# Performance work log

Hardware: AMD Instinct MI355X
Metric: run time of the kernel (lower is better)

The kernel has to match this reference:

```python
import jax, jax.numpy as jnp
import numpy as np

HEADS = 6
EPS = 1e-5

def conv1x1(x, w):
    return jax.lax.conv_general_dilated(x, w, (1, 1), 'VALID',
        dimension_numbers=('NCHW', 'OIHW', 'NCHW'))

def dwconv3x3(x, w):
    # depthwise 3x3, padding 1; w: [C,1,3,3]
    return jax.lax.conv_general_dilated(x, w, (1, 1), ((1, 1), (1, 1)),
        dimension_numbers=('NCHW', 'OIHW', 'NCHW'), feature_group_count=x.shape[1])

def layernorm(x, w, b):
    # WithBias LayerNorm over channel dim (applied per pixel)
    mu = x.mean(axis=1, keepdims=True)
    var = ((x - mu) ** 2).mean(axis=1, keepdims=True)
    return (x - mu) * jax.lax.rsqrt(var + EPS) * w[None, :, None, None] + b[None, :, None, None]

def l2norm(t):
    # matches torch F.normalize(dim=-1): norm clamped at 1e-12
    n = jnp.sqrt(jnp.sum(t * t, axis=-1, keepdims=True))
    return t / jnp.maximum(n, 1e-12)

def attention(x, f, qkv_w, dw_w, proj_w, temp):
    xin = x + f
    b, c, h, w = xin.shape
    qkv = dwconv3x3(conv1x1(xin, qkv_w), dw_w)
    q, k, v = jnp.split(qkv, 3, axis=1)
    hd = c // HEADS
    q = l2norm(q.reshape(b, HEADS, hd, h * w))
    k = l2norm(k.reshape(b, HEADS, hd, h * w))
    v = v.reshape(b, HEADS, hd, h * w)
    attn = jnp.einsum('bhcn,bhdn->bhcd', q, k) * temp[None]  # [b,H,hd,hd]
    attn = jax.nn.softmax(attn, axis=-1)
    out = jnp.einsum('bhcd,bhdn->bhcn', attn, v).reshape(b, c, h, w)
    return conv1x1(out, proj_w)

def ffn(x, in_w, dw_w, out_w):
    x = conv1x1(x, in_w)
    x1, x2 = jnp.split(dwconv3x3(x, dw_w), 2, axis=1)
    return conv1x1(jax.nn.gelu(x1, approximate=False) * x2, out_w)

def setup_inputs() -> dict:
    key = jax.random.key(0)
    B, C, H, W = 2, 96, 256, 256
    HID = int(C * 2.66)  # 255
    ks = jax.random.split(key, 32)
    p = lambda k, shp: (0.02 * jax.random.normal(k, shp, dtype=jnp.float32))
    d = {
        'Fw': jax.random.normal(ks[0], (B, C, H, W), dtype=jnp.float32),
        'F0_c': jax.random.normal(ks[1], (B, C, H, W), dtype=jnp.float32),
        'Kd': jax.random.normal(ks[2], (B, C, H, W), dtype=jnp.float32),
        'ln1_w': jnp.ones((C,), jnp.float32), 'ln1_b': jnp.zeros((C,), jnp.float32),
        'a1_qkv_w': p(ks[3], (3 * C, C, 1, 1)), 'a1_dw_w': p(ks[4], (3 * C, 1, 3, 3)),
        'a1_proj_w': p(ks[5], (C, C, 1, 1)), 'a1_temp': jnp.ones((HEADS, 1, 1), jnp.float32),
        'ln2_w': jnp.ones((C,), jnp.float32), 'ln2_b': jnp.zeros((C,), jnp.float32),
        'f1_in_w': p(ks[6], (2 * HID, C, 1, 1)), 'f1_dw_w': p(ks[7], (2 * HID, 1, 3, 3)),
        'f1_out_w': p(ks[8], (C, HID, 1, 1)),
        'ln3_w': jnp.ones((C,), jnp.float32), 'ln3_b': jnp.zeros((C,), jnp.float32),
        'a2_qkv_w': p(ks[9], (3 * C, C, 1, 1)), 'a2_dw_w': p(ks[10], (3 * C, 1, 3, 3)),
        'a2_proj_w': p(ks[11], (C, C, 1, 1)), 'a2_temp': jnp.ones((HEADS, 1, 1), jnp.float32),
        'ln4_w': jnp.ones((C,), jnp.float32), 'ln4_b': jnp.zeros((C,), jnp.float32),
        'f2_in_w': p(ks[12], (2 * HID, C, 1, 1)), 'f2_dw_w': p(ks[13], (2 * HID, 1, 3, 3)),
        'f2_out_w': p(ks[14], (C, HID, 1, 1)),
    }
    return d

def reference(Fw, F0_c, Kd, ln1_w, ln1_b, a1_qkv_w, a1_dw_w, a1_proj_w, a1_temp,
              ln2_w, ln2_b, f1_in_w, f1_dw_w, f1_out_w,
              ln3_w, ln3_b, a2_qkv_w, a2_dw_w, a2_proj_w, a2_temp,
              ln4_w, ln4_b, f2_in_w, f2_dw_w, f2_out_w):
    x = Fw + attention(layernorm(Fw, ln1_w, ln1_b), F0_c, a1_qkv_w, a1_dw_w, a1_proj_w, a1_temp)
    x = x + ffn(layernorm(x, ln2_w, ln2_b), f1_in_w, f1_dw_w, f1_out_w)
    x = x + attention(layernorm(x, ln3_w, ln3_b), Kd, a2_qkv_w, a2_dw_w, a2_proj_w, a2_temp)
    x = x + ffn(layernorm(x, ln4_w, ln4_b), f2_in_w, f2_dw_w, f2_out_w)
    return x
```

## Files before the change

### kernel.cpp

```cpp
#include <hip/hip_runtime.h>
#include <math.h>

using u16 = unsigned short;
using u32 = unsigned int;
typedef __attribute__((ext_vector_type(8))) short bf16x8;
typedef __attribute__((ext_vector_type(4))) float f32x4;
typedef __attribute__((ext_vector_type(16))) float f32x16;

#define NPLANE 65536
#define BELEMS ((size_t)6291456)
#define ASTR   ((size_t)33423360)
#define BSTR   ((size_t)18874368)

__device__ __forceinline__ float bf2f(u16 u) { return __uint_as_float(((u32)u) << 16); }
__device__ __forceinline__ u16 f2bf(float f) {
  if (!__builtin_isfinite(f)) return (u16)0x5F80;
  u32 u = __float_as_uint(f);
  return (u16)((u + 0x7fffu + ((u >> 16) & 1u)) >> 16);
}
__device__ __forceinline__ float4 cvt4(ushort4 v) {
  return make_float4(bf2f(v.x), bf2f(v.y), bf2f(v.z), bf2f(v.w));
}

union U16x8 { uint4 u4; bf16x8 v; u16 s[8]; };

__global__ void k_detect(const u16* __restrict__ p, u32* __restrict__ flag) {
  if (blockIdx.x == 0 && threadIdx.x == 0) *flag = (p[0] == (u16)0x3F80) ? 0u : 1u;
}

__device__ __forceinline__ float ldf(const void* p, int i, bool f32) {
  return f32 ? ((const float*)p)[i] : bf2f(((const u16*)p)[i]);
}

__global__ __launch_bounds__(256) void k_cvt_all(
    const void* p0, const void* p1, const void* p2, const void* p3,
    const void* p4, const void* p5, const void* p6, const void* p7,
    const void* p8, const void* p9, const void* p10, const void* p11,
    const void* p12, const void* p13, const void* p14, const void* p15,
    float* __restrict__ dst, const u32* __restrict__ fl)
{
  const int i = blockIdx.x * 256 + threadIdx.x;
  if (i >= 33576) return;
  const bool xf = (*fl != 0);
  const void* s; int o;
  if      (i < 2592)  { s = p0;  o = i; }
  else if (i < 7182)  { s = p1;  o = i - 2592; }
  else if (i < 9774)  { s = p2;  o = i - 7182; }
  else if (i < 14364) { s = p3;  o = i - 9774; }
  else if (i < 23580) { s = p4;  o = i - 14364; }
  else if (i < 32796) { s = p5;  o = i - 23580; }
  else if (i < 32802) { s = p6;  o = i - 32796; }
  else if (i < 32808) { s = p7;  o = i - 32802; }
  else if (i < 32904) { s = p8;  o = i - 32808; }
  else if (i < 33000) { s = p9;  o = i - 32904; }
  else if (i < 33096) { s = p10; o = i - 33000; }
  else if (i < 33192) { s = p11; o = i - 33096; }
  else if (i < 33288) { s = p12; o = i - 33192; }
  else if (i < 33384) { s = p13; o = i - 33288; }
  else if (i < 33480) { s = p14; o = i - 33384; }
  else                { s = p15; o = i - 33480; }
  dst[i] = ldf(s, o, xf);
}

__global__ __launch_bounds__(256) void k_wprep_all(
    const void* q1, const void* i1, const void* o1,
    const void* q2, const void* i2, const void* o2,
    u16* __restrict__ wbuf, const u32* __restrict__ fl)
{
  const int idx = blockIdx.x * 256 + threadIdx.x;
  if (idx >= 215040) return;
  const bool xf = (*fl != 0);
  const void* s; int local, M, Kr, Kpad;
  if      (idx < 27648)  { s = q1; local = idx;          M = 288; Kr = 96;  Kpad = 96;  }
  else if (idx < 82944)  { s = i1; local = idx - 27648;  M = 510; Kr = 96;  Kpad = 96;  }
  else if (idx < 107520) { s = o1; local = idx - 82944;  M = 96;  Kr = 255; Kpad = 256; }
  else if (idx < 135168) { s = q2; local = idx - 107520; M = 288; Kr = 96;  Kpad = 96;  }
  else if (idx < 190464) { s = i2; local = idx - 135168; M = 510; Kr = 96;  Kpad = 96;  }
  else                   { s = o2; local = idx - 190464; M = 96;  Kr = 255; Kpad = 256; }
  const int m = local / Kpad, k = local - m * Kpad;
  u16 v = 0;
  if (m < M && k < Kr) v = f2bf(ldf(s, m * Kr + k, xf));
  wbuf[idx] = v;
}

__global__ __launch_bounds__(256) void k_lnp(
    const void* __restrict__ x, const u32* __restrict__ xfl,
    const void* __restrict__ f, const u32* __restrict__ ffl,
    const float* __restrict__ lnw, const float* __restrict__ lnb,
    u16* __restrict__ xT)
{
  __shared__ float xin[96 * 64];
  __shared__ float fin[96 * 64];
  __shared__ float ps[256], pq[256];
  __shared__ float mu[64], rsd[64];
  const int tid = threadIdx.x;
  const int pix0 = blockIdx.x * 64;
  const int z = blockIdx.z;
  const size_t eb = (size_t)z * BELEMS;
  u16* xTo = xT + (size_t)z * BSTR;
  const bool xf = xfl && (*xfl != 0);
  const bool ff = ffl && (*ffl != 0);

#pragma unroll
  for (int i = 0; i < 6; ++i) {
    const int u = tid + i * 256;
    const int c = u >> 4, p4 = (u & 15) << 2;
    const size_t base = eb + (size_t)c * NPLANE + pix0 + p4;
    const float4 v = xf ? *(const float4*)((const float*)x + base)
                        : cvt4(*(const ushort4*)((const u16*)x + base));
    *(float4*)(xin + c * 64 + p4) = v;
    if (f) {
      const float4 fv = ff ? *(const float4*)((const float*)f + base)
                           : cvt4(*(const ushort4*)((const u16*)f + base));
      *(float4*)(fin + c * 64 + p4) = fv;
    }
  }
  __syncthreads();
  {
    const int p = tid & 63, qq = tid >> 6;
    float s = 0.f, q = 0.f;
    const int c0 = qq * 24;
#pragma unroll 8
    for (int c = c0; c < c0 + 24; ++c) {
      const float v = xin[c * 64 + p];
      s += v; q += v * v;
    }
    ps[tid] = s; pq[tid] = q;
  }
  __syncthreads();
  if (tid < 64) {
    const float s = ps[tid] + ps[tid + 64] + ps[tid + 128] + ps[tid + 192];
    const float q = pq[tid] + pq[tid + 64] + pq[tid + 128] + pq[tid + 192];
    const float m = s * (1.f / 96.f);
    mu[tid] = m;
    rsd[tid] = rsqrtf(fmaxf(q * (1.f / 96.f) - m * m, 0.f) + 1e-5f);
  }
  __syncthreads();
#pragma unroll
  for (int i = 0; i < 6; ++i) {
    const int u = tid + i * 256;
    const int c = u >> 4, p4 = (u & 15) << 2;
    const float4 v = *(const float4*)(xin + c * 64 + p4);
    const float w = lnw[c], b = lnb[c];
    float o0 = (v.x - mu[p4 + 0]) * rsd[p4 + 0] * w + b;
    float o1 = (v.y - mu[p4 + 1]) * rsd[p4 + 1] * w + b;
    float o2 = (v.z - mu[p4 + 2]) * rsd[p4 + 2] * w + b;
    float o3 = (v.w - mu[p4 + 3]) * rsd[p4 + 3] * w + b;
    if (f) {
      const float4 fv = *(const float4*)(fin + c * 64 + p4);
      o0 += fv.x; o1 += fv.y; o2 += fv.z; o3 += fv.w;
    }
    *(float4*)(xin + c * 64 + p4) = make_float4(o0, o1, o2, o3);
  }
  __syncthreads();
#pragma unroll
  for (int i = 0; i < 3; ++i) {
    const int u = tid + i * 256;
    const int px = u / 12, q = u - px * 12;
    U16x8 pk;
#pragma unroll
    for (int e = 0; e < 8; ++e) pk.s[e] = f2bf(xin[(q * 8 + e) * 64 + px]);
    *(uint4*)(xTo + (size_t)(pix0 + px) * 96 + q * 8) = pk.u4;
  }
}

__global__ __launch_bounds__(256) void k_gemm_bt(
    const u16* __restrict__ BT, size_t bts, const u16* __restrict__ A,
    int OC, u16* __restrict__ out, size_t ots)
{
  __shared__ u16 Bs[128 * 104];
  const int t = threadIdx.x;
  const int oc0 = blockIdx.x * 96;
  const int n0 = blockIdx.y * 128;
  const int z = blockIdx.z;
  const u16* BTz = BT + (size_t)z * bts;
  u16* outz = out + (size_t)z * ots;
  const int l = t & 63, wid = t >> 6, wm = wid >> 1, wn = wid & 1;

  const uint4* src = (const uint4*)(BTz + (size_t)n0 * 96);
#pragma unroll
  for (int i = 0; i < 6; ++i) {
    const int u = t + i * 256;
    const int r = u / 12, q = u - r * 12;
    *(uint4*)(Bs + r * 104 + q * 8) = src[u];
  }
  __syncthreads();

  f32x4 acc[3][4];
#pragma unroll
  for (int m = 0; m < 3; ++m)
#pragma unroll
    for (int n = 0; n < 4; ++n) acc[m][n] = (f32x4){0.f, 0.f, 0.f, 0.f};

#pragma unroll
  for (int ks = 0; ks < 3; ++ks) {
    const int kk = (ks << 5) + ((l >> 4) << 3);
    U16x8 a[3], b[4];
#pragma unroll
    for (int m = 0; m < 3; ++m)
      a[m].u4 = *(const uint4*)(A + (size_t)(oc0 + wm * 48 + m * 16 + (l & 15)) * 96 + kk);
#pragma unroll
    for (int ns = 0; ns < 4; ++ns)
      b[ns].u4 = *(const uint4*)(Bs + (wn * 64 + ns * 16 + (l & 15)) * 104 + kk);
#pragma unroll
    for (int m = 0; m < 3; ++m)
#pragma unroll
      for (int ns = 0; ns < 4; ++ns)
        acc[m][ns] = __builtin_amdgcn_mfma_f32_16x16x32_bf16(a[m].v, b[ns].v, acc[m][ns], 0, 0, 0);
  }

  __syncthreads();
  u16* ct = Bs;
#pragma unroll
  for (int m = 0; m < 3; ++m) {
    const int rl = wm * 48 + m * 16 + ((l >> 4) << 2);
#pragma unroll
    for (int ns = 0; ns < 4; ++ns) {
      const int nl = wn * 64 + ns * 16 + (l & 15);
#pragma unroll
      for (int r = 0; r < 4; ++r) ct[(rl + r) * 136 + nl] = f2bf(acc[m][ns][r]);
    }
  }
  __syncthreads();
#pragma unroll
  for (int i = 0; i < 6; ++i) {
    const int u = t + i * 256;
    const int r = u >> 4, q = u & 15;
    if (oc0 + r < OC) {
      const uint4 pk = *(const uint4*)(ct + r * 136 + q * 8);
      *(uint4*)(outz + (size_t)(oc0 + r) * NPLANE + n0 + q * 8) = pk;
    }
  }
}

__global__ __launch_bounds__(256) void k_gemm(
    const u16* __restrict__ xsrc, size_t xzs, const u16* __restrict__ A, int azs,
    int K, int Kpad, int OC,
    const void* __restrict__ res, const u32* __restrict__ rfl,
    void* __restrict__ out, const u32* __restrict__ ofl)
{
  __shared__ uint4 Bt[128 * 16];
  const int t = threadIdx.x;
  const int p = t & 127, h = t >> 7;
  const int oc0 = blockIdx.x * 96;
  const int n0 = blockIdx.y * 128;
  const int z = blockIdx.z;
  const u16* xz = xsrc + (size_t)z * xzs;
  const u16* Az = A + (size_t)z * (size_t)azs;
  const size_t eb = (size_t)z * BELEMS;
  const int nglob = n0 + p;
  const int l = t & 63, wid = t >> 6, wm = wid >> 1, wn = wid & 1;

  f32x4 acc[3][4];
#pragma unroll
  for (int m = 0; m < 3; ++m)
#pragma unroll
    for (int n = 0; n < 4; ++n) acc[m][n] = (f32x4){0.f, 0.f, 0.f, 0.f};

  for (int kb = 0; kb < K; kb += 128) {
    if (kb) __syncthreads();
    const int kc = min(128, K - kb);
    const int U = (kc + 7) >> 3;
    const int uh = U >> 1;
    for (int j = 0; j < uh; ++j) {
      const int u = h * uh + j;
      const int cb = kb + u * 8;
      U16x8 pk;
#pragma unroll
      for (int e = 0; e < 8; ++e) {
        const int c = cb + e;
        pk.s[e] = (c < K) ? xz[(size_t)c * NPLANE + nglob] : (u16)0;
      }
      Bt[p * 16 + (u ^ (p & 7))] = pk.u4;
    }
    __syncthreads();
    const int nks = (kc + 31) >> 5;
    for (int ks = 0; ks < nks; ++ks) {
      U16x8 a[3], b[4];
      const int kk = kb + ks * 32 + ((l >> 4) << 3);
#pragma unroll
      for (int m = 0; m < 3; ++m) {
        const int row = oc0 + wm * 48 + m * 16 + (l & 15);
        a[m].u4 = ((const uint4*)Az)[((size_t)row * Kpad + kk) >> 3];
      }
#pragma unroll
      for (int ns = 0; ns < 4; ++ns) {
        const int row = wn * 64 + ns * 16 + (l & 15);
        const int up = (ks * 4 + (l >> 4)) ^ (row & 7);
        b[ns].u4 = Bt[row * 16 + up];
      }
#pragma unroll
      for (int m = 0; m < 3; ++m)
#pragma unroll
        for (int ns = 0; ns < 4; ++ns)
          acc[m][ns] = __builtin_amdgcn_mfma_f32_16x16x32_bf16(a[m].v, b[ns].v, acc[m][ns], 0, 0, 0);
    }
  }

  const bool rf = rfl && (*rfl != 0);
  const bool of = ofl && (*ofl != 0);
#pragma unroll
  for (int m = 0; m < 3; ++m) {
    const int ocb = oc0 + wm * 48 + m * 16 + ((l >> 4) << 2);
#pragma unroll
    for (int ns = 0; ns < 4; ++ns) {
      const int n = n0 + wn * 64 + ns * 16 + (l & 15);
#pragma unroll
      for (int r = 0; r < 4; ++r) {
        const int oc = ocb + r;
        if (oc < OC) {
          float v = acc[m][ns][r];
          const size_t gi = eb + (size_t)oc * NPLANE + n;
          if (res) v += rf ? ((const float*)res)[gi] : bf2f(((const u16*)res)[gi]);
          if (of) ((float*)out)[gi] = v;
          else    ((u16*)out)[gi] = f2bf(v);
        }
      }
    }
  }
}

__global__ __launch_bounds__(256) void k_dw(
    const u16* __restrict__ in, const float* __restrict__ w9, u16* __restrict__ out)
{
  const int c = blockIdx.y;
  const int r0 = blockIdx.x * 16;
  const int z = blockIdx.z;
  __shared__ float tt[18 * 256];
  const int tid = threadIdx.x;
  const u16* ip = in + (size_t)z * ASTR + (size_t)c * NPLANE;
  for (int u = tid; u < 1152; u += 256) {
    const int r = u >> 6, p4 = (u & 63) << 2;
    const int gr = r0 - 1 + r;
    float4 fv = make_float4(0.f, 0.f, 0.f, 0.f);
    if (gr >= 0 && gr < 256) fv = cvt4(*(const ushort4*)(ip + gr * 256 + p4));
    *(float4*)(tt + r * 256 + p4) = fv;
  }
  float wr[9];
#pragma unroll
  for (int i = 0; i < 9; ++i) wr[i] = w9[c * 9 + i];
  __syncthreads();
  const int col = tid;
  const bool cm = col > 0, cp = col < 255;
  float a0 = cm ? tt[col - 1] : 0.f, a1 = tt[col], a2 = cp ? tt[col + 1] : 0.f;
  float b0 = cm ? tt[256 + col - 1] : 0.f, b1 = tt[256 + col], b2 = cp ? tt[256 + col + 1] : 0.f;
  u16* op = out + (size_t)z * BSTR + (size_t)c * NPLANE + (size_t)r0 * 256 + col;
#pragma unroll
  for (int rr = 0; rr < 16; ++rr) {
    const int rn = (rr + 2) * 256;
    const float c1 = tt[rn + col];
    const float c0 = cm ? tt[rn + col - 1] : 0.f;
    const float c2 = cp ? tt[rn + col + 1] : 0.f;
    const float s = wr[0] * a0 + wr[1] * a1 + wr[2] * a2
                  + wr[3] * b0 + wr[4] * b1 + wr[5] * b2
                  + wr[6] * c0 + wr[7] * c1 + wr[8] * c2;
    op[rr * 256] = f2bf(s);
    a0 = b0; a1 = b1; a2 = b2; b0 = c0; b1 = c1; b2 = c2;
  }
}

__global__ __launch_bounds__(256) void k_dw_gelu(
    const u16* __restrict__ in, const float* __restrict__ w9, u16* __restrict__ out)
{
  const int c = blockIdx.y;
  const int r0 = blockIdx.x * 16;
  const int z = blockIdx.z;
  __shared__ float t1[18 * 256];
  __shared__ float t2[18 * 256];
  const int tid = threadIdx.x;
  const u16* ip1 = in + (size_t)z * ASTR + (size_t)c * NPLANE;
  const u16* ip2 = in + (size_t)z * ASTR + (size_t)(c + 255) * NPLANE;
  for (int u = tid; u < 1152; u += 256) {
    const int r = u >> 6, p4 = (u & 63) << 2;
    const int gr = r0 - 1 + r;
    float4 fa = make_float4(0.f, 0.f, 0.f, 0.f), fb = fa;
    if (gr >= 0 && gr < 256) {
      fa = cvt4(*(const ushort4*)(ip1 + gr * 256 + p4));
      fb = cvt4(*(const ushort4*)(ip2 + gr * 256 + p4));
    }
    *(float4*)(t1 + r * 256 + p4) = fa;
    *(float4*)(t2 + r * 256 + p4) = fb;
  }
  float wa[9], wb9[9];
#pragma unroll
  for (int i = 0; i < 9; ++i) { wa[i] = w9[c * 9 + i]; wb9[i] = w9[(c + 255) * 9 + i]; }
  __syncthreads();
  const int col = tid;
  const bool cm = col > 0, cp = col < 255;
  float a0 = cm ? t1[col - 1] : 0.f, a1 = t1[col], a2 = cp ? t1[col + 1] : 0.f;
  float b0 = cm ? t1[256 + col - 1] : 0.f, b1 = t1[256 + col], b2 = cp ? t1[256 + col + 1] : 0.f;
  float d0 = cm ? t2[col - 1] : 0.f, d1 = t2[col], d2 = cp ? t2[col + 1] : 0.f;
  float e0 = cm ? t2[256 + col - 1] : 0.f, e1 = t2[256 + col], e2 = cp ? t2[256 + col + 1] : 0.f;
  u16* op = out + (size_t)z * BSTR + (size_t)c * NPLANE + (size_t)r0 * 256 + col;
#pragma unroll
  for (int rr = 0; rr < 16; ++rr) {
    const int rn = (rr + 2) * 256;
    const float c1 = t1[rn + col];
    const float c0 = cm ? t1[rn + col - 1] : 0.f;
    const float c2 = cp ? t1[rn + col + 1] : 0.f;
    const float g1 = wa[0] * a0 + wa[1] * a1 + wa[2] * a2
                   + wa[3] * b0 + wa[4] * b1 + wa[5] * b2
                   + wa[6] * c0 + wa[7] * c1 + wa[8] * c2;
    const float f1 = t2[rn + col];
    const float f0 = cm ? t2[rn + col - 1] : 0.f;
    const float f2 = cp ? t2[rn + col + 1] : 0.f;
    const float g2 = wb9[0] * d0 + wb9[1] * d1 + wb9[2] * d2
                   + wb9[3] * e0 + wb9[4] * e1 + wb9[5] * e2
                   + wb9[6] * f0 + wb9[7] * f1 + wb9[8] * f2;
    const float gel = 0.5f * g1 * (1.f + erff(g1 * 0.70710678118654752f));
    op[rr * 256] = f2bf(gel * g2);
    a0 = b0; a1 = b1; a2 = b2; b0 = c0; b1 = c1; b2 = c2;
    d0 = e0; d1 = e1; d2 = e2; e0 = f0; e1 = f1; e2 = f2;
  }
}

__global__ __launch_bounds__(256) void k_reduce_s(
    const u16* __restrict__ qkv, float* __restrict__ S,
    float* __restrict__ qn2, float* __restrict__ kn2)
{
  const int h = blockIdx.y;
  const int n0 = blockIdx.x * 512;
  const int zb = blockIdx.z;
  const u16* qz = qkv + (size_t)zb * BSTR;
  float* Sz = S + zb * 1728;
  float* qn2z = qn2 + zb * 1728;
  float* kn2z = kn2 + zb * 1728;
  __shared__ uint4 st[64 * 33];
  const int tid = threadIdx.x;
  const int l = tid & 63, w = tid >> 6;

#pragma unroll
  for (int i = 0; i < 8; ++i) {
    const int idx = tid + i * 256;
    const int c = idx & 63, r = idx >> 6;
    const int plane = (r < 16) ? (h * 16 + r) : (96 + h * 16 + (r - 16));
    st[c * 33 + r] = *(const uint4*)(qz + (size_t)plane * NPLANE + n0 + c * 8);
  }
  __syncthreads();

  f32x16 acc;
#pragma unroll
  for (int j = 0; j < 16; ++j) acc[j] = 0.f;
  const int row = l & 31;
  const int cg = (w << 4) + (l >> 5);
#pragma unroll
  for (int s = 0; s < 8; ++s) {
    U16x8 frag;
    frag.u4 = st[(cg + s * 2) * 33 + row];
    acc = __builtin_amdgcn_mfma_f32_32x32x16_bf16(frag.v, frag.v, acc, 0, 0, 0);
  }
  __syncthreads();

  float* fs = (float*)st;
#pragma unroll
  for (int j = 0; j < 16; ++j) {
    const int rj = (j & 3) + 8 * (j >> 2) + 4 * (l >> 5);
    fs[w * 1024 + rj * 32 + (l & 31)] = acc[j];
  }
  __syncthreads();
#pragma unroll
  for (int e4 = 0; e4 < 4; ++e4) {
    const int e = tid * 4 + e4;
    const float v = fs[e] + fs[1024 + e] + fs[2048 + e] + fs[3072 + e];
    const int r = e >> 5, cc = e & 31;
    if (r < 16 && cc >= 16) atomicAdd(Sz + h * 256 + r * 16 + (cc - 16), v);
    if (r == cc) {
      if (r < 16) atomicAdd(qn2z + h * 16 + r, v);
      else        atomicAdd(kn2z + h * 16 + (r - 16), v);
    }
  }
}

__global__ __launch_bounds__(256) void k_softmax_m(
    const float* __restrict__ S, const float* __restrict__ qn2, const float* __restrict__ kn2,
    const float* __restrict__ temp, const float* __restrict__ proj, u16* __restrict__ Mtb)
{
  __shared__ float attn[6 * 256];
  const int tid = threadIdx.x;
  const int zb = blockIdx.z;
  const float* Sz = S + zb * 1728;
  const float* qn2z = qn2 + zb * 1728;
  const float* kn2z = kn2 + zb * 1728;
  u16* Mz = Mtb + zb * 9216;
  if (tid < 96) {
    const int h = tid >> 4, i = tid & 15;
    const float qn = fmaxf(sqrtf(qn2z[tid]), 1e-12f);
    const float tp = temp[h];
    float row[16];
    float mx = -3.4e38f;
#pragma unroll
    for (int d = 0; d < 16; ++d) {
      const float kn = fmaxf(sqrtf(kn2z[h * 16 + d]), 1e-12f);
      row[d] = Sz[h * 256 + i * 16 + d] / (qn * kn) * tp;
      mx = fmaxf(mx, row[d]);
    }
    float sum = 0.f;
#pragma unroll
    for (int d = 0; d < 16; ++d) { row[d] = expf(row[d] - mx); sum += row[d]; }
    const float inv = 1.f / sum;
#pragma unroll
    for (int d = 0; d < 16; ++d) attn[h * 256 + i * 16 + d] = row[d] * inv;
  }
  __syncthreads();
  for (int u = tid; u < 9216; u += 256) {
    const int e = u / 96, dg = u - e * 96;
    const int h = dg >> 4, d = dg & 15;
    float s = 0.f;
#pragma unroll
    for (int i = 0; i < 16; ++i)
      s += proj[e * 96 + h * 16 + i] * attn[h * 256 + i * 16 + d];
    Mz[u] = f2bf(s);
  }
}

extern "C" void kernel_launch(void* const* d_in, const int* in_sizes, int n_in,
                              void* d_out, int out_size, void* d_ws, size_t ws_size,
                              hipStream_t stream)
{
  (void)in_sizes; (void)n_in; (void)out_size;
  if (ws_size < (size_t)234975000) return;

  const void* Fw  = d_in[0];
  const void* F0c = d_in[1];
  const void* Kdi = d_in[2];

  char* ws = (char*)d_ws;
  u16* xcur = (u16*)ws;
  u16* bufA = (u16*)(ws + 25165824);
  u16* bufB = (u16*)(ws + 158859264);
  u16* wb   = (u16*)(ws + 234356736);
  u16* Wq1 = wb;           u16* Wi1 = wb + 27648;   u16* Wo1 = wb + 82944;
  u16* Wq2 = wb + 107520;  u16* Wi2 = wb + 135168;  u16* Wo2 = wb + 190464;
  u16* Mtb = wb + 215040;
  float* fz = (float*)(ws + 234823680);
  float* dwA1 = fz;          float* dwF1 = fz + 2592;
  float* dwA2 = fz + 7182;   float* dwF2 = fz + 9774;
  float* prj1 = fz + 14364;  float* prj2 = fz + 23580;
  float* tmp1 = fz + 32796;  float* tmp2 = fz + 32802;
  float* lnp  = fz + 32808;
  float* Sb   = fz + 33576;
  float* Qn   = Sb + 1536;
  float* Kn   = Sb + 1632;
  u32*  flag  = (u32*)(fz + 37032);

  k_detect<<<1, 64, 0, stream>>>((const u16*)d_in[3], flag);

  k_wprep_all<<<dim3(840), 256, 0, stream>>>(d_in[5], d_in[11], d_in[13],
                                             d_in[16], d_in[22], d_in[24], wb, flag);
  k_cvt_all<<<dim3(132), 256, 0, stream>>>(
      d_in[6], d_in[12], d_in[17], d_in[23], d_in[7], d_in[18], d_in[8], d_in[19],
      d_in[3], d_in[4], d_in[9], d_in[10], d_in[14], d_in[15], d_in[20], d_in[21],
      fz, flag);

  auto attn_stage = [&](const void* x, const u32* xfl, const void* f, const u32* ffl,
                        const float* lw, const float* lb, const u16* Wq,
                        const float* dwf, const float* tmpf, const float* prjf,
                        const void* res, const u32* rfl,
                        void* outx, const u32* ofl) {
    hipMemsetAsync(Sb, 0, 2 * 1728 * sizeof(float), stream);
    k_lnp<<<dim3(1024, 1, 2), 256, 0, stream>>>(x, xfl, f, ffl, lw, lb, bufB);
    k_gemm_bt<<<dim3(3, 512, 2), 256, 0, stream>>>(bufB, BSTR, Wq, 288, bufA, ASTR);
    k_dw<<<dim3(16, 288, 2), 256, 0, stream>>>(bufA, dwf, bufB);
    k_reduce_s<<<dim3(128, 6, 2), 256, 0, stream>>>(bufB, Sb, Qn, Kn);
    k_softmax_m<<<dim3(1, 1, 2), 256, 0, stream>>>(Sb, Qn, Kn, tmpf, prjf, Mtb);
    k_gemm<<<dim3(1, 512, 2), 256, 0, stream>>>(bufB + (size_t)192 * NPLANE, BSTR,
                                                Mtb, 9216, 96, 96, 96,
                                                res, rfl, outx, ofl);
  };
  auto ffn_stage = [&](const void* x, const u32* xfl,
                       const float* lw, const float* lb, const u16* Wi,
                       const float* dwf, const u16* Wo,
                       void* outx, const u32* ofl) {
    k_lnp<<<dim3(1024, 1, 2), 256, 0, stream>>>(x, xfl, nullptr, nullptr, lw, lb, bufB);
    k_gemm_bt<<<dim3(6, 512, 2), 256, 0, stream>>>(bufB, BSTR, Wi, 510, bufA, ASTR);
    k_dw_gelu<<<dim3(16, 255, 2), 256, 0, stream>>>(bufA, dwf, bufB);
    k_gemm<<<dim3(1, 512, 2), 256, 0, stream>>>(bufB, BSTR, Wo, 0, 255, 256, 96,
                                                x, xfl, outx, ofl);
  };

  attn_stage(Fw, flag, F0c, flag, lnp + 0, lnp + 96, Wq1, dwA1, tmp1, prj1,
             Fw, flag, xcur, nullptr);
  ffn_stage(xcur, nullptr, lnp + 192, lnp + 288, Wi1, dwF1, Wo1, xcur, nullptr);
  attn_stage(xcur, nullptr, Kdi, flag, lnp + 384, lnp + 480, Wq2, dwA2, tmp2, prj2,
             xcur, nullptr, xcur, nullptr);
  ffn_stage(xcur, nullptr, lnp + 576, lnp + 672, Wi2, dwF2, Wo2, d_out, flag);
}
```

Measured before the change: 744.0 us.

## Compute two columns per thread in depthwise convs and use tanh GELU

Both depthwise 3x3 kernels now give each thread two adjacent output columns over half the rows. This reuses shared-memory neighbour loads across the pair and writes packed 32-bit bf16 stores. The FFN gate also swaps the exact erf GELU for a tanh approximation built on __expf, which cuts special-function cost. The reference uses approximate=False, so the tanh form brings a small numeric deviation that bf16 output precision may or may not absorb.

```diff
diff --git a/kernel.cpp b/kernel.cpp
--- a/kernel.cpp
+++ b/kernel.cpp
@@ -20,6 +20,12 @@
 }
 __device__ __forceinline__ float4 cvt4(ushort4 v) {
   return make_float4(bf2f(v.x), bf2f(v.y), bf2f(v.z), bf2f(v.w));
+}
+__device__ __forceinline__ float gelu_f(float x) {
+  const float y = 0.7978845608f * x * (1.f + 0.044715f * x * x);
+  const float e = __expf(-2.f * fabsf(y));
+  const float th = __builtin_copysignf((1.f - e) / (1.f + e), y);
+  return 0.5f * x * (1.f + th);
 }
 
 union U16x8 { uint4 u4; bf16x8 v; u16 s[8]; };
@@ -340,22 +346,32 @@
 #pragma unroll
   for (int i = 0; i < 9; ++i) wr[i] = w9[c * 9 + i];
   __syncthreads();
-  const int col = tid;
-  const bool cm = col > 0, cp = col < 255;
-  float a0 = cm ? tt[col - 1] : 0.f, a1 = tt[col], a2 = cp ? tt[col + 1] : 0.f;
-  float b0 = cm ? tt[256 + col - 1] : 0.f, b1 = tt[256 + col], b2 = cp ? tt[256 + col + 1] : 0.f;
-  u16* op = out + (size_t)z * BSTR + (size_t)c * NPLANE + (size_t)r0 * 256 + col;
-#pragma unroll
-  for (int rr = 0; rr < 16; ++rr) {
-    const int rn = (rr + 2) * 256;
-    const float c1 = tt[rn + col];
-    const float c0 = cm ? tt[rn + col - 1] : 0.f;
-    const float c2 = cp ? tt[rn + col + 1] : 0.f;
-    const float s = wr[0] * a0 + wr[1] * a1 + wr[2] * a2
-                  + wr[3] * b0 + wr[4] * b1 + wr[5] * b2
-                  + wr[6] * c0 + wr[7] * c1 + wr[8] * c2;
-    op[rr * 256] = f2bf(s);
-    a0 = b0; a1 = b1; a2 = b2; b0 = c0; b1 = c1; b2 = c2;
+  const int cp = tid & 127, rh = tid >> 7;
+  const int cl = cp << 1;
+  const bool cm = cp > 0, cpk = cp < 127;
+  const int rb = rh << 3;
+  float a0 = cm ? tt[rb * 256 + cl - 1] : 0.f;
+  float a1 = tt[rb * 256 + cl], a2 = tt[rb * 256 + cl + 1];
+  float a3 = cpk ? tt[rb * 256 + cl + 2] : 0.f;
+  float b0 = cm ? tt[(rb + 1) * 256 + cl - 1] : 0.f;
+  float b1 = tt[(rb + 1) * 256 + cl], b2 = tt[(rb + 1) * 256 + cl + 1];
+  float b3 = cpk ? tt[(rb + 1) * 256 + cl + 2] : 0.f;
+  u16* op = out + (size_t)z * BSTR + (size_t)c * NPLANE + (size_t)(r0 + rb) * 256 + cl;
+#pragma unroll
+  for (int rr = 0; rr < 8; ++rr) {
+    const int rn = (rb + 2 + rr) * 256;
+    const float c0 = cm ? tt[rn + cl - 1] : 0.f;
+    const float c1 = tt[rn + cl], c2 = tt[rn + cl + 1];
+    const float c3 = cpk ? tt[rn + cl + 2] : 0.f;
+    const float o0 = wr[0] * a0 + wr[1] * a1 + wr[2] * a2
+                   + wr[3] * b0 + wr[4] * b1 + wr[5] * b2
+                   + wr[6] * c0 + wr[7] * c1 + wr[8] * c2;
+    const float o1 = wr[0] * a1 + wr[1] * a2 + wr[2] * a3
+                   + wr[3] * b1 + wr[4] * b2 + wr[5] * b3
+                   + wr[6] * c1 + wr[7] * c2 + wr[8] * c3;
+    *(u32*)(op + rr * 256) = (u32)f2bf(o0) | ((u32)f2bf(o1) << 16);
+    a0 = b0; a1 = b1; a2 = b2; a3 = b3;
+    b0 = c0; b1 = c1; b2 = c2; b3 = c3;
   }
 }
 
@@ -381,36 +397,55 @@
     *(float4*)(t1 + r * 256 + p4) = fa;
     *(float4*)(t2 + r * 256 + p4) = fb;
   }
-  float wa[9], wb9[9];
-#pragma unroll
-  for (int i = 0; i < 9; ++i) { wa[i] = w9[c * 9 + i]; wb9[i] = w9[(c + 255) * 9 + i]; }
-  __syncthreads();
-  const int col = tid;
-  const bool cm = col > 0, cp = col < 255;
-  float a0 = cm ? t1[col - 1] : 0.f, a1 = t1[col], a2 = cp ? t1[col + 1] : 0.f;
-  float b0 = cm ? t1[256 + col - 1] : 0.f, b1 = t1[256 + col], b2 = cp ? t1[256 + col + 1] : 0.f;
-  float d0 = cm ? t2[col - 1] : 0.f, d1 = t2[col], d2 = cp ? t2[col + 1] : 0.f;
-  float e0 = cm ? t2[256 + col - 1] : 0.f, e1 = t2[256 + col], e2 = cp ? t2[256 + col + 1] : 0.f;
-  u16* op = out + (size_t)z * BSTR + (size_t)c * NPLANE + (size_t)r0 * 256 + col;
-#pragma unroll
-  for (int rr = 0; rr < 16; ++rr) {
-    const int rn = (rr + 2) * 256;
-    const float c1 = t1[rn + col];
-    const float c0 = cm ? t1[rn + col - 1] : 0.f;
-    const float c2 = cp ? t1[rn + col + 1] : 0.f;
-    const float g1 = wa[0] * a0 + wa[1] * a1 + wa[2] * a2
-                   + wa[3] * b0 + wa[4] * b1 + wa[5] * b2
-                   + wa[6] * c0 + wa[7] * c1 + wa[8] * c2;
-    const float f1 = t2[rn + col];
-    const float f0 = cm ? t2[rn + col - 1] : 0.f;
-    const float f2 = cp ? t2[rn + col + 1] : 0.f;
-    const float g2 = wb9[0] * d0 + wb9[1] * d1 + wb9[2] * d2
-                   + wb9[3] * e0 + wb9[4] * e1 + wb9[5] * e2
-                   + wb9[6] * f0 + wb9[7] * f1 + wb9[8] * f2;
-    const float gel = 0.5f * g1 * (1.f + erff(g1 * 0.70710678118654752f));
-    op[rr * 256] = f2bf(gel * g2);
-    a0 = b0; a1 = b1; a2 = b2; b0 = c0; b1 = c1; b2 = c2;
-    d0 = e0; d1 = e1; d2 = e2; e0 = f0; e1 = f1; e2 = f2;
+  float wa[9], wb[9];
+#pragma unroll
+  for (int i = 0; i < 9; ++i) { wa[i] = w9[c * 9 + i]; wb[i] = w9[(c + 255) * 9 + i]; }
+  __syncthreads();
+  const int cp = tid & 127, rh = tid >> 7;
+  const int cl = cp << 1;
+  const bool cm = cp > 0, cpk = cp < 127;
+  const int rb = rh << 3;
+  float a0 = cm ? t1[rb * 256 + cl - 1] : 0.f;
+  float a1 = t1[rb * 256 + cl], a2 = t1[rb * 256 + cl + 1];
+  float a3 = cpk ? t1[rb * 256 + cl + 2] : 0.f;
+  float b0 = cm ? t1[(rb + 1) * 256 + cl - 1] : 0.f;
+  float b1 = t1[(rb + 1) * 256 + cl], b2 = t1[(rb + 1) * 256 + cl + 1];
+  float b3 = cpk ? t1[(rb + 1) * 256 + cl + 2] : 0.f;
+  float d0 = cm ? t2[rb * 256 + cl - 1] : 0.f;
+  float d1 = t2[rb * 256 + cl], d2 = t2[rb * 256 + cl + 1];
+  float d3 = cpk ? t2[rb * 256 + cl + 2] : 0.f;
+  float e0 = cm ? t2[(rb + 1) * 256 + cl - 1] : 0.f;
+  float e1 = t2[(rb + 1) * 256 + cl], e2 = t2[(rb + 1) * 256 + cl + 1];
+  float e3 = cpk ? t2[(rb + 1) * 256 + cl + 2] : 0.f;
+  u16* op = out + (size_t)z * BSTR + (size_t)c * NPLANE + (size_t)(r0 + rb) * 256 + cl;
+#pragma unroll
+  for (int rr = 0; rr < 8; ++rr) {
+    const int rn = (rb + 2 + rr) * 256;
+    const float c0 = cm ? t1[rn + cl - 1] : 0.f;
+    const float c1 = t1[rn + cl], c2 = t1[rn + cl + 1];
+    const float c3 = cpk ? t1[rn + cl + 2] : 0.f;
+    const float f0 = cm ? t2[rn + cl - 1] : 0.f;
+    const float f1 = t2[rn + cl], f2 = t2[rn + cl + 1];
+    const float f3 = cpk ? t2[rn + cl + 2] : 0.f;
+    const float g10 = wa[0] * a0 + wa[1] * a1 + wa[2] * a2
+                    + wa[3] * b0 + wa[4] * b1 + wa[5] * b2
+                    + wa[6] * c0 + wa[7] * c1 + wa[8] * c2;
+    const float g11 = wa[0] * a1 + wa[1] * a2 + wa[2] * a3
+                    + wa[3] * b1 + wa[4] * b2 + wa[5] * b3
+                    + wa[6] * c1 + wa[7] * c2 + wa[8] * c3;
+    const float g20 = wb[0] * d0 + wb[1] * d1 + wb[2] * d2
+                    + wb[3] * e0 + wb[4] * e1 + wb[5] * e2
+                    + wb[6] * f0 + wb[7] * f1 + wb[8] * f2;
+    const float g21 = wb[0] * d1 + wb[1] * d2 + wb[2] * d3
+                    + wb[3] * e1 + wb[4] * e2 + wb[5] * e3
+                    + wb[6] * f1 + wb[7] * f2 + wb[8] * f3;
+    const float o0 = gelu_f(g10) * g20;
+    const float o1 = gelu_f(g11) * g21;
+    *(u32*)(op + rr * 256) = (u32)f2bf(o0) | ((u32)f2bf(o1) << 16);
+    a0 = b0; a1 = b1; a2 = b2; a3 = b3;
+    b0 = c0; b1 = c1; b2 = c2; b3 = c3;
+    d0 = e0; d1 = e1; d2 = e2; d3 = e3;
+    e0 = f0; e1 = f1; e2 = f2; e3 = f3;
   }
 }
 
```

After: 736.9 us (median of 2 runs). No clear change (-1.0%).

## Fuse FFN LayerNorm into attention projection GEMM epilogue, use tanh GELU

Applied to the files above, without the earlier changes.

The attention output-projection GEMM now stages its result tile in shared memory, writes the residual output, and computes the per-pixel channel LayerNorm for the following FFN. It writes the normalized pixel-major tensor directly into the FFN input buffer, which removes a separate k_lnp launch and its re-read of the activation. The LayerNorm uses the sum/sum-of-squares variance form on bf16-rounded values. Separately, the exact erf GELU is replaced by the tanh approximation using fast exp, which changes numerics slightly to cut transcendental cost in the depthwise kernel.

```diff
diff --git a/kernel.cpp b/kernel.cpp
--- a/kernel.cpp
+++ b/kernel.cpp
@@ -20,6 +20,12 @@
 }
 __device__ __forceinline__ float4 cvt4(ushort4 v) {
   return make_float4(bf2f(v.x), bf2f(v.y), bf2f(v.z), bf2f(v.w));
+}
+__device__ __forceinline__ float gelu_f(float x) {
+  const float y = 0.7978845608f * x * (1.f + 0.044715f * x * x);
+  const float e = __expf(-2.f * fabsf(y));
+  const float th = __builtin_copysignf((1.f - e) / (1.f + e), y);
+  return 0.5f * x * (1.f + th);
 }
 
 union U16x8 { uint4 u4; bf16x8 v; u16 s[8]; };
@@ -237,9 +243,12 @@
     const u16* __restrict__ xsrc, size_t xzs, const u16* __restrict__ A, int azs,
     int K, int Kpad, int OC,
     const void* __restrict__ res, const u32* __restrict__ rfl,
-    void* __restrict__ out, const u32* __restrict__ ofl)
+    void* __restrict__ out, const u32* __restrict__ ofl,
+    const float* __restrict__ lnw, const float* __restrict__ lnb,
+    u16* __restrict__ xT, size_t xts)
 {
   __shared__ uint4 Bt[128 * 16];
+  __shared__ float ps[256], pq[256], mu[128], rsd[128];
   const int t = threadIdx.x;
   const int p = t & 127, h = t >> 7;
   const int oc0 = blockIdx.x * 96;
@@ -298,25 +307,91 @@
   }
 
   const bool rf = rfl && (*rfl != 0);
-  const bool of = ofl && (*ofl != 0);
-#pragma unroll
-  for (int m = 0; m < 3; ++m) {
-    const int ocb = oc0 + wm * 48 + m * 16 + ((l >> 4) << 2);
-#pragma unroll
-    for (int ns = 0; ns < 4; ++ns) {
-      const int n = n0 + wn * 64 + ns * 16 + (l & 15);
-#pragma unroll
-      for (int r = 0; r < 4; ++r) {
-        const int oc = ocb + r;
-        if (oc < OC) {
-          float v = acc[m][ns][r];
-          const size_t gi = eb + (size_t)oc * NPLANE + n;
-          if (res) v += rf ? ((const float*)res)[gi] : bf2f(((const u16*)res)[gi]);
-          if (of) ((float*)out)[gi] = v;
-          else    ((u16*)out)[gi] = f2bf(v);
+  if (xT == nullptr) {
+    const bool of = ofl && (*ofl != 0);
+#pragma unroll
+    for (int m = 0; m < 3; ++m) {
+      const int ocb = oc0 + wm * 48 + m * 16 + ((l >> 4) << 2);
+#pragma unroll
+      for (int ns = 0; ns < 4; ++ns) {
+        const int n = n0 + wn * 64 + ns * 16 + (l & 15);
+#pragma unroll
+        for (int r = 0; r < 4; ++r) {
+          const int oc = ocb + r;
+          if (oc < OC) {
+            float v = acc[m][ns][r];
+            const size_t gi = eb + (size_t)oc * NPLANE + n;
+            if (res) v += rf ? ((const float*)res)[gi] : bf2f(((const u16*)res)[gi]);
+            if (of) ((float*)out)[gi] = v;
+            else    ((u16*)out)[gi] = f2bf(v);
+          }
         }
       }
     }
+    return;
+  }
+
+  __syncthreads();
+  u16* ct = (u16*)Bt;
+#pragma unroll
+  for (int m = 0; m < 3; ++m) {
+    const int rl = wm * 48 + m * 16 + ((l >> 4) << 2);
+#pragma unroll
+    for (int ns = 0; ns < 4; ++ns) {
+      const int nl = wn * 64 + ns * 16 + (l & 15);
+      const int n = n0 + nl;
+#pragma unroll
+      for (int r = 0; r < 4; ++r) {
+        float v = acc[m][ns][r];
+        const size_t gi = eb + (size_t)(rl + r) * NPLANE + n;
+        if (res) v += rf ? ((const float*)res)[gi] : bf2f(((const u16*)res)[gi]);
+        ct[(rl + r) * 136 + nl] = f2bf(v);
+      }
+    }
+  }
+  __syncthreads();
+  u16* outz = (u16*)out + eb;
+#pragma unroll
+  for (int i = 0; i < 6; ++i) {
+    const int u = t + i * 256;
+    const int r = u >> 4, q = u & 15;
+    const uint4 pk = *(const uint4*)(ct + r * 136 + q * 8);
+    *(uint4*)(outz + (size_t)r * NPLANE + n0 + q * 8) = pk;
+  }
+  {
+    const int px = p, half = h;
+    float s = 0.f, q2 = 0.f;
+    const int c0 = half * 48;
+#pragma unroll 8
+    for (int c = c0; c < c0 + 48; ++c) {
+      const float v = bf2f(ct[c * 136 + px]);
+      s += v; q2 += v * v;
+    }
+    ps[t] = s; pq[t] = q2;
+  }
+  __syncthreads();
+  if (t < 128) {
+    const float s = ps[t] + ps[t + 128];
+    const float q2 = pq[t] + pq[t + 128];
+    const float m = s * (1.f / 96.f);
+    mu[t] = m;
+    rsd[t] = rsqrtf(fmaxf(q2 * (1.f / 96.f) - m * m, 0.f) + 1e-5f);
+  }
+  __syncthreads();
+  u16* xTz = xT + (size_t)z * xts;
+#pragma unroll
+  for (int i = 0; i < 6; ++i) {
+    const int u = t + i * 256;
+    const int row = u / 12, q = u - row * 12;
+    const float m = mu[row], rs = rsd[row];
+    U16x8 pk;
+#pragma unroll
+    for (int e = 0; e < 8; ++e) {
+      const int c = q * 8 + e;
+      const float v = bf2f(ct[c * 136 + row]);
+      pk.s[e] = f2bf((v - m) * rs * lnw[c] + lnb[c]);
+    }
+    *(uint4*)(xTz + (size_t)(n0 + row) * 96 + q * 8) = pk.u4;
   }
 }
 
@@ -407,8 +482,7 @@
     const float g2 = wb9[0] * d0 + wb9[1] * d1 + wb9[2] * d2
                    + wb9[3] * e0 + wb9[4] * e1 + wb9[5] * e2
                    + wb9[6] * f0 + wb9[7] * f1 + wb9[8] * f2;
-    const float gel = 0.5f * g1 * (1.f + erff(g1 * 0.70710678118654752f));
-    op[rr * 256] = f2bf(gel * g2);
+    op[rr * 256] = f2bf(gelu_f(g1) * g2);
     a0 = b0; a1 = b1; a2 = b2; b0 = c0; b1 = c1; b2 = c2;
     d0 = e0; d1 = e1; d2 = e2; e0 = f0; e1 = f1; e2 = f2;
   }
@@ -556,7 +630,8 @@
                         const float* lw, const float* lb, const u16* Wq,
                         const float* dwf, const float* tmpf, const float* prjf,
                         const void* res, const u32* rfl,
-                        void* outx, const u32* ofl) {
+                        void* outx, const u32* ofl,
+                        const float* nlw, const float* nlb) {
     hipMemsetAsync(Sb, 0, 2 * 1728 * sizeof(float), stream);
     k_lnp<<<dim3(1024, 1, 2), 256, 0, stream>>>(x, xfl, f, ffl, lw, lb, bufB);
     k_gemm_bt<<<dim3(3, 512, 2), 256, 0, stream>>>(bufB, BSTR, Wq, 288, bufA, ASTR);
@@ -565,23 +640,23 @@
     k_softmax_m<<<dim3(1, 1, 2), 256, 0, stream>>>(Sb, Qn, Kn, tmpf, prjf, Mtb);
     k_gemm<<<dim3(1, 512, 2), 256, 0, stream>>>(bufB + (size_t)192 * NPLANE, BSTR,
                                                 Mtb, 9216, 96, 96, 96,
-                                                res, rfl, outx, ofl);
+                                                res, rfl, outx, ofl,
+                                                nlw, nlb, bufB, BSTR);
   };
   auto ffn_stage = [&](const void* x, const u32* xfl,
-                       const float* lw, const float* lb, const u16* Wi,
-                       const float* dwf, const u16* Wo,
+                       const u16* Wi, const float* dwf, const u16* Wo,
                        void* outx, const u32* ofl) {
-    k_lnp<<<dim3(1024, 1, 2), 256, 0, stream>>>(x, xfl, nullptr, nullptr, lw, lb, bufB);
     k_gemm_bt<<<dim3(6, 512, 2), 256, 0, stream>>>(bufB, BSTR, Wi, 510, bufA, ASTR);
     k_dw_gelu<<<dim3(16, 255, 2), 256, 0, stream>>>(bufA, dwf, bufB);
     k_gemm<<<dim3(1, 512, 2), 256, 0, stream>>>(bufB, BSTR, Wo, 0, 255, 256, 96,
-                                                x, xfl, outx, ofl);
+                                                x, xfl, outx, ofl,
+                                                nullptr, nullptr, nullptr, 0);
   };
 
   attn_stage(Fw, flag, F0c, flag, lnp + 0, lnp + 96, Wq1, dwA1, tmp1, prj1,
-             Fw, flag, xcur, nullptr);
-  ffn_stage(xcur, nullptr, lnp + 192, lnp + 288, Wi1, dwF1, Wo1, xcur, nullptr);
+             Fw, flag, xcur, nullptr, lnp + 192, lnp + 288);
+  ffn_stage(xcur, nullptr, Wi1, dwF1, Wo1, xcur, nullptr);
   attn_stage(xcur, nullptr, Kdi, flag, lnp + 384, lnp + 480, Wq2, dwA2, tmp2, prj2,
-             xcur, nullptr, xcur, nullptr);
-  ffn_stage(xcur, nullptr, lnp + 576, lnp + 672, Wi2, dwF2, Wo2, d_out, flag);
-}
+             xcur, nullptr, xcur, nullptr, lnp + 576, lnp + 672);
+  ffn_stage(xcur, nullptr, Wi2, dwF2, Wo2, d_out, flag);
+}
```

Result: slower. 792.3 us (+6.5%).
